# Kernel optimization log

Hardware: AMD Instinct MI355X
Metric: run time of the kernel (lower is better)

Reference implementation:

```python
import jax, jax.numpy as jnp
import numpy as np

D_MODEL = 1024

def setup_inputs() -> dict:
    key = jax.random.key(0)
    ks = jax.random.split(key, 7)
    x = jax.random.normal(ks[0], (4, 4096, D_MODEL), dtype=jnp.float32)
    s = 1.0 / np.sqrt(D_MODEL)
    Wq = jax.random.uniform(ks[1], (D_MODEL, D_MODEL), jnp.float32, -s, s)
    bq = jax.random.uniform(ks[2], (D_MODEL,), jnp.float32, -s, s)
    Wk = jax.random.uniform(ks[3], (D_MODEL, D_MODEL), jnp.float32, -s, s)
    bk = jax.random.uniform(ks[4], (D_MODEL,), jnp.float32, -s, s)
    Wv = jax.random.uniform(ks[5], (D_MODEL, D_MODEL), jnp.float32, -s, s)
    bv = jax.random.uniform(ks[6], (D_MODEL,), jnp.float32, -s, s)
    return {"x": x, "Wq": Wq, "bq": bq, "Wk": Wk, "bk": bk, "Wv": Wv, "bv": bv}

def reference(x, Wq, bq, Wk, bk, Wv, bv):
    # Q, K, V: [b, s, d]
    Q = jnp.einsum('bsd,ed->bse', x, Wq) + bq
    K = jnp.einsum('bsd,ed->bse', x, Wk) + bk
    V = jnp.einsum('bsd,ed->bse', x, Wv) + bv
    scale = 1.0 / jnp.sqrt(jnp.asarray(D_MODEL, dtype=x.dtype))
    scores = jnp.einsum('bqd,bkd->bqk', Q, K) * scale  # [b, s, s]
    attn = jax.nn.softmax(scores, axis=-1)
    return jnp.einsum('bqk,bkd->bqd', attn, V)
```

## Files before the change

### kernel.cpp

```cpp
#include <hip/hip_runtime.h>
#include <stdint.h>
#include <stddef.h>

#define DM 1024
#define SEQ 4096
#define NB 4
#define NTOK (NB*SEQ)

typedef __attribute__((ext_vector_type(8))) short s16x8;
typedef __attribute__((ext_vector_type(4))) float f32x4;

__device__ __forceinline__ unsigned short f2bf(float f) {
  unsigned int u = __float_as_uint(f);
  u += 0x7FFFu + ((u >> 16) & 1u);
  return (unsigned short)(u >> 16);
}
__device__ __forceinline__ float bf2f(unsigned short u) {
  return __uint_as_float((unsigned int)u << 16);
}

__device__ __forceinline__ f32x4 mfma16(s16x8 a, s16x8 b, f32x4 c) {
  return __builtin_amdgcn_mfma_f32_16x16x32_bf16(a, b, c, 0, 0, 0);
}

__device__ __forceinline__ void gload16(const void* g, void* l) {
  __builtin_amdgcn_global_load_lds((const __attribute__((address_space(1))) unsigned int*)g,
                                   (__attribute__((address_space(3))) unsigned int*)l, 16, 0, 0);
}

__device__ __forceinline__ void xcd_swz(int gx, int gy, int& x, int& y, int& z) {
  int nwg = gx * gy * gridDim.z;
  int bid = blockIdx.x + gx * (blockIdx.y + gy * blockIdx.z);
  int cpx = nwg >> 3;
  int wg = (bid & 7) * cpx + (bid >> 3);
  x = wg % gx; int t = wg / gx; y = t % gy; z = t / gy;
}

__global__ void k_conv(const float* __restrict__ s, unsigned short* __restrict__ d, int n8) {
  int i = blockIdx.x * blockDim.x + threadIdx.x;
  int st = gridDim.x * blockDim.x;
  for (; i < n8; i += st) {
    const f32x4* sp = (const f32x4*)s + (size_t)i * 2;
    f32x4 a = sp[0], b = sp[1];
    s16x8 o;
    o[0] = (short)f2bf(a[0]); o[1] = (short)f2bf(a[1]);
    o[2] = (short)f2bf(a[2]); o[3] = (short)f2bf(a[3]);
    o[4] = (short)f2bf(b[0]); o[5] = (short)f2bf(b[1]);
    o[6] = (short)f2bf(b[2]); o[7] = (short)f2bf(b[3]);
    *((s16x8*)d + i) = o;
  }
}

template<int KD, int BK, int EPI>
__device__ __forceinline__ void gemm_core(
    const unsigned short* __restrict__ A, const unsigned short* __restrict__ B,
    void* __restrict__ outp, int ldc, const float* __restrict__ aux, float scale,
    int mbase, int nbase)
{
  constexpr int NT     = KD / BK;
  constexpr int SLOTS  = BK / 8;
  constexpr int SMASK  = SLOTS - 1;
  constexpr int PASSES = 128 * SLOTS / 256;

  __shared__ unsigned short lds[2][2][128 * BK];
  const int tid = threadIdx.x, lane = tid & 63, wid = tid >> 6;
  const int wr = wid >> 1, wc = wid & 1;
  const int l15 = lane & 15, lg = lane >> 4;

  f32x4 acc[4][4];
  #pragma unroll
  for (int m = 0; m < 4; m++)
    #pragma unroll
    for (int n = 0; n < 4; n++) { acc[m][n][0]=0.f; acc[m][n][1]=0.f; acc[m][n][2]=0.f; acc[m][n][3]=0.f; }

  auto rswz = [](int row) -> int { return (BK == 64) ? (row & 7) : ((row >> 1) & 3); };

  auto stage = [&](int buf, int kt) {
    const int kb_ = kt * BK;
    #pragma unroll
    for (int p = 0; p < PASSES; p++) {
      int s = p * 256 + tid;
      int row = s / SLOTS, sl = (s & SMASK) ^ rswz(row);
      gload16(A + (size_t)(mbase + row) * KD + kb_ + sl * 8, &lds[buf][0][s * 8]);
    }
    #pragma unroll
    for (int p = 0; p < PASSES; p++) {
      int s = p * 256 + tid;
      int row = s / SLOTS, sl = (s & SMASK) ^ rswz(row);
      gload16(B + (size_t)(nbase + row) * KD + kb_ + sl * 8, &lds[buf][1][s * 8]);
    }
  };

  auto compute = [&](int buf) {
    #pragma unroll
    for (int k2 = 0; k2 < BK / 32; k2++) {
      s16x8 af[4], bf[4];
      #pragma unroll
      for (int m = 0; m < 4; m++) {
        int row = wr * 64 + m * 16 + l15;
        int sl = (k2 * 4 + lg) ^ rswz(row);
        af[m] = *(const s16x8*)(&lds[buf][0][0] + row * BK + sl * 8);
      }
      #pragma unroll
      for (int n = 0; n < 4; n++) {
        int row = wc * 64 + n * 16 + l15;
        int sl = (k2 * 4 + lg) ^ rswz(row);
        bf[n] = *(const s16x8*)(&lds[buf][1][0] + row * BK + sl * 8);
      }
      #pragma unroll
      for (int m = 0; m < 4; m++)
        #pragma unroll
        for (int n = 0; n < 4; n++)
          acc[m][n] = mfma16(af[m], bf[n], acc[m][n]);
    }
  };

  stage(0, 0);
  __syncthreads();
  for (int kt = 0; kt < NT; kt++) {
    int cur = kt & 1;
    if (kt < NT - 1) stage(cur ^ 1, kt + 1);
    compute(cur);
    __syncthreads();
  }

  #pragma unroll
  for (int n = 0; n < 4; n++) {
    int col = nbase + wc * 64 + n * 16 + l15;
    float cb = (EPI == 0) ? aux[col] : 0.f;
    #pragma unroll
    for (int m = 0; m < 4; m++) {
      #pragma unroll
      for (int r = 0; r < 4; r++) {
        int row = mbase + wr * 64 + m * 16 + lg * 4 + r;
        float v = acc[m][n][r];
        if (EPI == 0) {
          ((unsigned short*)outp)[(size_t)row * ldc + col] = f2bf(v + cb);
        } else if (EPI == 1) {
          ((unsigned short*)outp)[(size_t)row * ldc + col] = f2bf(__expf(v * scale));
        } else if (EPI == 3) {
          ((unsigned short*)outp)[(size_t)row * ldc + col] = f2bf(v + aux[row]);
        } else {
          ((float*)outp)[(size_t)row * ldc + col] = v * aux[row];
        }
      }
    }
  }
}

__global__ __launch_bounds__(256, 4) void k_qkv(
    const unsigned short* __restrict__ xb, const unsigned short* __restrict__ wb,
    const float* __restrict__ b0, const float* __restrict__ b1, const float* __restrict__ bv,
    unsigned short* __restrict__ qo, unsigned short* __restrict__ ko, unsigned short* __restrict__ vt)
{
  int x, y, z;
  xcd_swz(8, 128, x, y, z);
  if (z < 2) {
    gemm_core<DM, 32, 0>(xb, wb + (size_t)z * DM * DM,
                         z ? ko : qo, DM, z ? b1 : b0, 0.f,
                         y * 128, x * 128);
  } else {
    int batch = y >> 5, tokb = (y & 31) * 128;
    gemm_core<DM, 32, 3>(wb + (size_t)2 * DM * DM, xb + (size_t)batch * SEQ * DM,
                         vt + (size_t)batch * DM * SEQ, SEQ, bv, 0.f,
                         x * 128, tokb);
  }
}

__global__ __launch_bounds__(256, 4) void k_sgemm(
    const unsigned short* __restrict__ qb, const unsigned short* __restrict__ kb,
    unsigned short* __restrict__ sc0, unsigned short* __restrict__ sc1, int bb)
{
  int x, y, z;
  xcd_swz(32, 32, x, y, z);
  gemm_core<DM, 32, 1>(qb + (size_t)(bb + z) * SEQ * DM, kb + (size_t)(bb + z) * SEQ * DM,
                       z ? sc1 : sc0, SEQ, nullptr, 0.03125f,
                       y * 128, x * 128);
}

__global__ __launch_bounds__(256) void k_rowsum(const unsigned short* __restrict__ sc0,
                                                const unsigned short* __restrict__ sc1,
                                                float* __restrict__ linv) {
  const unsigned short* sc = blockIdx.z ? sc1 : sc0;
  const int row = blockIdx.x * 4 + (threadIdx.x >> 6);
  const int lane = threadIdx.x & 63;
  const unsigned short* rp = sc + (size_t)row * SEQ + lane * 8;
  float s = 0.f;
  #pragma unroll
  for (int j = 0; j < 8; j++) {
    s16x8 v = *(const s16x8*)(rp + (size_t)j * 512);
    #pragma unroll
    for (int t = 0; t < 8; t++) s += bf2f((unsigned short)v[t]);
  }
  s += __shfl_xor(s, 1);  s += __shfl_xor(s, 2);  s += __shfl_xor(s, 4);
  s += __shfl_xor(s, 8);  s += __shfl_xor(s, 16); s += __shfl_xor(s, 32);
  if (lane == 0) linv[blockIdx.z * SEQ + row] = 1.f / s;
}

__global__ __launch_bounds__(256, 2) void k_pv(
    const unsigned short* __restrict__ sc0, const unsigned short* __restrict__ sc1,
    const unsigned short* __restrict__ vt, const float* __restrict__ linv,
    float* __restrict__ out, int bb)
{
  int x, y, z;
  xcd_swz(8, 32, x, y, z);
  gemm_core<SEQ, 64, 4>(z ? sc1 : sc0, vt + (size_t)(bb + z) * DM * SEQ,
                        out + (size_t)(bb + z) * SEQ * DM, DM, linv + z * SEQ, 1.f,
                        y * 128, x * 128);
}

extern "C" void kernel_launch(void* const* d_in, const int* in_sizes, int n_in,
                              void* d_out, int out_size, void* d_ws, size_t ws_size,
                              hipStream_t stream) {
  const float* x  = (const float*)d_in[0];
  const float* Wq = (const float*)d_in[1];
  const float* bq = (const float*)d_in[2];
  const float* Wk = (const float*)d_in[3];
  const float* bk = (const float*)d_in[4];
  const float* Wv = (const float*)d_in[5];
  const float* bv = (const float*)d_in[6];
  float* out = (float*)d_out;
  char* ws = (char*)d_ws;

  unsigned short* xb = (unsigned short*)(ws);
  unsigned short* wb = (unsigned short*)(ws + 33554432);
  unsigned short* qb = (unsigned short*)(ws + 39845888);
  unsigned short* kb = (unsigned short*)(ws + 73400320);
  unsigned short* sc1 = (unsigned short*)(ws + 106954752);
  unsigned short* vt = (unsigned short*)(ws + 140509184);
  float* linv = (float*)(ws + 174063616);
  unsigned short* sc0 = xb;

  k_conv<<<4096, 256, 0, stream>>>(x, xb, NTOK * DM / 8);
  k_conv<<<512, 256, 0, stream>>>(Wq, wb, DM * DM / 8);
  k_conv<<<512, 256, 0, stream>>>(Wk, wb + DM * DM, DM * DM / 8);
  k_conv<<<512, 256, 0, stream>>>(Wv, wb + 2 * DM * DM, DM * DM / 8);

  k_qkv<<<dim3(8, 128, 3), 256, 0, stream>>>(xb, wb, bq, bk, bv, qb, kb, vt);

  for (int bb = 0; bb < NB; bb += 2) {
    k_sgemm<<<dim3(32, 32, 2), 256, 0, stream>>>(qb, kb, sc0, sc1, bb);
    k_rowsum<<<dim3(1024, 1, 2), 256, 0, stream>>>(sc0, sc1, linv);
    k_pv<<<dim3(8, 32, 2), 256, 0, stream>>>(sc0, sc1, vt, linv, out, bb);
  }
}
```

Before: 511.6 us.

## Process all four batches in single attention launches when workspace allows

When the workspace is large enough, the score GEMM, row-sum and PV kernels now run over all four batches in one launch each, using two extra score buffers, instead of looping over batch pairs. This doubles the grid of each launch, which should improve CU fill and tail behaviour and removes three kernel launches. In that path the PV GEMM also uses a 32-wide K tile with occupancy hint 4 instead of 64 with 2. The change costs more workspace memory and falls back to the old two-batch loop if the workspace is too small.

```diff
diff --git a/kernel.cpp b/kernel.cpp
--- a/kernel.cpp
+++ b/kernel.cpp
@@ -53,6 +53,7 @@
 
 template<int KD, int BK, int EPI>
 __device__ __forceinline__ void gemm_core(
+    unsigned short (*lds)[2][128 * BK],
     const unsigned short* __restrict__ A, const unsigned short* __restrict__ B,
     void* __restrict__ outp, int ldc, const float* __restrict__ aux, float scale,
     int mbase, int nbase)
@@ -62,7 +63,6 @@
   constexpr int SMASK  = SLOTS - 1;
   constexpr int PASSES = 128 * SLOTS / 256;
 
-  __shared__ unsigned short lds[2][2][128 * BK];
   const int tid = threadIdx.x, lane = tid & 63, wid = tid >> 6;
   const int wr = wid >> 1, wc = wid & 1;
   const int l15 = lane & 15, lg = lane >> 4;
@@ -153,15 +153,16 @@
     const float* __restrict__ b0, const float* __restrict__ b1, const float* __restrict__ bv,
     unsigned short* __restrict__ qo, unsigned short* __restrict__ ko, unsigned short* __restrict__ vt)
 {
+  __shared__ unsigned short lds[2][2][128 * 32];
   int x, y, z;
   xcd_swz(8, 128, x, y, z);
   if (z < 2) {
-    gemm_core<DM, 32, 0>(xb, wb + (size_t)z * DM * DM,
+    gemm_core<DM, 32, 0>(lds, xb, wb + (size_t)z * DM * DM,
                          z ? ko : qo, DM, z ? b1 : b0, 0.f,
                          y * 128, x * 128);
   } else {
     int batch = y >> 5, tokb = (y & 31) * 128;
-    gemm_core<DM, 32, 3>(wb + (size_t)2 * DM * DM, xb + (size_t)batch * SEQ * DM,
+    gemm_core<DM, 32, 3>(lds, wb + (size_t)2 * DM * DM, xb + (size_t)batch * SEQ * DM,
                          vt + (size_t)batch * DM * SEQ, SEQ, bv, 0.f,
                          x * 128, tokb);
   }
@@ -169,19 +170,24 @@
 
 __global__ __launch_bounds__(256, 4) void k_sgemm(
     const unsigned short* __restrict__ qb, const unsigned short* __restrict__ kb,
-    unsigned short* __restrict__ sc0, unsigned short* __restrict__ sc1, int bb)
-{
+    unsigned short* __restrict__ s0, unsigned short* __restrict__ s1,
+    unsigned short* __restrict__ s2, unsigned short* __restrict__ s3, int bb)
+{
+  __shared__ unsigned short lds[2][2][128 * 32];
   int x, y, z;
   xcd_swz(32, 32, x, y, z);
-  gemm_core<DM, 32, 1>(qb + (size_t)(bb + z) * SEQ * DM, kb + (size_t)(bb + z) * SEQ * DM,
-                       z ? sc1 : sc0, SEQ, nullptr, 0.03125f,
+  unsigned short* sc = (z == 0) ? s0 : (z == 1) ? s1 : (z == 2) ? s2 : s3;
+  gemm_core<DM, 32, 1>(lds, qb + (size_t)(bb + z) * SEQ * DM, kb + (size_t)(bb + z) * SEQ * DM,
+                       sc, SEQ, nullptr, 0.03125f,
                        y * 128, x * 128);
 }
 
-__global__ __launch_bounds__(256) void k_rowsum(const unsigned short* __restrict__ sc0,
-                                                const unsigned short* __restrict__ sc1,
-                                                float* __restrict__ linv) {
-  const unsigned short* sc = blockIdx.z ? sc1 : sc0;
+__global__ __launch_bounds__(256) void k_rowsum(
+    const unsigned short* __restrict__ s0, const unsigned short* __restrict__ s1,
+    const unsigned short* __restrict__ s2, const unsigned short* __restrict__ s3,
+    float* __restrict__ linv, int bb) {
+  const int z = blockIdx.z;
+  const unsigned short* sc = (z == 0) ? s0 : (z == 1) ? s1 : (z == 2) ? s2 : s3;
   const int row = blockIdx.x * 4 + (threadIdx.x >> 6);
   const int lane = threadIdx.x & 63;
   const unsigned short* rp = sc + (size_t)row * SEQ + lane * 8;
@@ -194,18 +200,23 @@
   }
   s += __shfl_xor(s, 1);  s += __shfl_xor(s, 2);  s += __shfl_xor(s, 4);
   s += __shfl_xor(s, 8);  s += __shfl_xor(s, 16); s += __shfl_xor(s, 32);
-  if (lane == 0) linv[blockIdx.z * SEQ + row] = 1.f / s;
-}
-
-__global__ __launch_bounds__(256, 2) void k_pv(
-    const unsigned short* __restrict__ sc0, const unsigned short* __restrict__ sc1,
+  if (lane == 0) linv[(size_t)(bb + z) * SEQ + row] = 1.f / s;
+}
+
+template<int BK>
+__global__ __launch_bounds__(256, (BK == 32) ? 4 : 2) void k_pv(
+    const unsigned short* __restrict__ s0, const unsigned short* __restrict__ s1,
+    const unsigned short* __restrict__ s2, const unsigned short* __restrict__ s3,
     const unsigned short* __restrict__ vt, const float* __restrict__ linv,
     float* __restrict__ out, int bb)
 {
+  __shared__ unsigned short lds[2][2][128 * BK];
   int x, y, z;
   xcd_swz(8, 32, x, y, z);
-  gemm_core<SEQ, 64, 4>(z ? sc1 : sc0, vt + (size_t)(bb + z) * DM * SEQ,
-                        out + (size_t)(bb + z) * SEQ * DM, DM, linv + z * SEQ, 1.f,
+  const unsigned short* sc = (z == 0) ? s0 : (z == 1) ? s1 : (z == 2) ? s2 : s3;
+  gemm_core<SEQ, BK, 4>(lds, sc, vt + (size_t)(bb + z) * DM * SEQ,
+                        out + (size_t)(bb + z) * SEQ * DM, DM,
+                        linv + (size_t)(bb + z) * SEQ, 1.f,
                         y * 128, x * 128);
 }
 
@@ -222,14 +233,17 @@
   float* out = (float*)d_out;
   char* ws = (char*)d_ws;
 
-  unsigned short* xb = (unsigned short*)(ws);
-  unsigned short* wb = (unsigned short*)(ws + 33554432);
-  unsigned short* qb = (unsigned short*)(ws + 39845888);
-  unsigned short* kb = (unsigned short*)(ws + 73400320);
+  unsigned short* xb  = (unsigned short*)(ws);
+  unsigned short* wb  = (unsigned short*)(ws + 33554432);
+  unsigned short* qb  = (unsigned short*)(ws + 39845888);
+  unsigned short* kb  = (unsigned short*)(ws + 73400320);
   unsigned short* sc1 = (unsigned short*)(ws + 106954752);
-  unsigned short* vt = (unsigned short*)(ws + 140509184);
-  float* linv = (float*)(ws + 174063616);
+  unsigned short* vt  = (unsigned short*)(ws + 140509184);
+  float* linv         = (float*)(ws + 174063616);
   unsigned short* sc0 = xb;
+  unsigned short* sc2 = (unsigned short*)(ws + 174129152);
+  unsigned short* sc3 = (unsigned short*)(ws + 207683584);
+  const bool big = ws_size >= 241238016ull;
 
   k_conv<<<4096, 256, 0, stream>>>(x, xb, NTOK * DM / 8);
   k_conv<<<512, 256, 0, stream>>>(Wq, wb, DM * DM / 8);
@@ -238,9 +252,15 @@
 
   k_qkv<<<dim3(8, 128, 3), 256, 0, stream>>>(xb, wb, bq, bk, bv, qb, kb, vt);
 
-  for (int bb = 0; bb < NB; bb += 2) {
-    k_sgemm<<<dim3(32, 32, 2), 256, 0, stream>>>(qb, kb, sc0, sc1, bb);
-    k_rowsum<<<dim3(1024, 1, 2), 256, 0, stream>>>(sc0, sc1, linv);
-    k_pv<<<dim3(8, 32, 2), 256, 0, stream>>>(sc0, sc1, vt, linv, out, bb);
-  }
-}
+  if (big) {
+    k_sgemm<<<dim3(32, 32, 4), 256, 0, stream>>>(qb, kb, sc0, sc1, sc2, sc3, 0);
+    k_rowsum<<<dim3(1024, 1, 4), 256, 0, stream>>>(sc0, sc1, sc2, sc3, linv, 0);
+    k_pv<32><<<dim3(8, 32, 4), 256, 0, stream>>>(sc0, sc1, sc2, sc3, vt, linv, out, 0);
+  } else {
+    for (int bb = 0; bb < NB; bb += 2) {
+      k_sgemm<<<dim3(32, 32, 2), 256, 0, stream>>>(qb, kb, sc0, sc1, sc0, sc1, bb);
+      k_rowsum<<<dim3(1024, 1, 2), 256, 0, stream>>>(sc0, sc1, sc0, sc1, linv, bb);
+      k_pv<64><<<dim3(8, 32, 2), 256, 0, stream>>>(sc0, sc1, sc0, sc1, vt, linv, out, bb);
+    }
+  }
+}
```

After: 508.5 us. No clear change (-0.6%).
